# Optimization experiments

Measured on AMD Instinct MI355X. Metric: run time of the kernel, lower is better.

Reference implementation:

```python
import jax, jax.numpy as jnp
import numpy as np

K = 20  # neighbors per point (module default)


def _knn_idx(x, k):
    # x: [N, d] -> indices of k nearest points (self included, as in torch_cluster.knn)
    d2 = jnp.sum(x * x, axis=-1)
    dist = d2[:, None] + d2[None, :] - 2.0 * (x @ x.T)  # [N, N] squared distances
    _, idx = jax.lax.top_k(-dist, k)  # smallest distances
    return idx  # [N, k]


def _mlp(h, layers):
    # layers: list of (W, b, relu_flag); BN is identity (eval mode, fresh running stats)
    for W, b, relu in layers:
        h = h @ W + b
        if relu:
            h = jax.nn.relu(h)
    return h


def _dynamic_edge_conv(x, layers, k=K):
    # x: [B, N, d]; dynamic kNN graph per graph, edge feat [x_i, x_j - x_i], MLP, max-aggr
    idx = jax.vmap(lambda xx: _knn_idx(jax.lax.stop_gradient(xx), k))(x)  # [B, N, k]
    xj = jax.vmap(lambda xx, ii: xx[ii])(x, idx)  # [B, N, k, d] neighbor gather
    xi = x[:, :, None, :]
    feat = jnp.concatenate([jnp.broadcast_to(xi, xj.shape), xj - xi], axis=-1)  # [B,N,k,2d]
    return jnp.max(_mlp(feat, layers), axis=2)  # [B, N, d_out]


def setup_inputs() -> dict:
    key = jax.random.key(0)
    ks = jax.random.split(key, 20)
    s = 0.05
    B, N, PD, OUT = 8, 4096, 2, 10
    f32 = jnp.float32

    def w(k, shape):
        return jax.random.normal(k, shape, dtype=f32) * s

    return {
        "data": jax.random.normal(ks[0], (B, N, PD), dtype=f32),
        # conv1 MLP: [2*PD, 64, 64, 64]
        "c1w1": w(ks[1], (2 * PD, 64)), "c1b1": jnp.zeros((64,), f32),
        "c1w2": w(ks[2], (64, 64)),     "c1b2": jnp.zeros((64,), f32),
        "c1w3": w(ks[3], (64, 64)),     "c1b3": jnp.zeros((64,), f32),
        # conv2 MLP: [2*64, 128]
        "c2w1": w(ks[4], (128, 128)),   "c2b1": jnp.zeros((128,), f32),
        # lin1: 192 -> 1024
        "lin1_w": w(ks[5], (192, 1024)), "lin1_b": jnp.zeros((1024,), f32),
        # head MLP: [1024, 512, 256, OUT]
        "mw1": w(ks[6], (1024, 512)), "mb1": jnp.zeros((512,), f32),
        "mw2": w(ks[7], (512, 256)),  "mb2": jnp.zeros((256,), f32),
        "mw3": w(ks[8], (256, OUT)),  "mb3": jnp.zeros((OUT,), f32),
    }


def reference(data, c1w1, c1b1, c1w2, c1b2, c1w3, c1b3, c2w1, c2b1,
              lin1_w, lin1_b, mw1, mb1, mw2, mb2, mw3, mb3):
    # DynamicEdgeConv 1: MLP([4,64,64,64]) (plain last layer)
    x1 = _dynamic_edge_conv(data, [(c1w1, c1b1, True), (c1w2, c1b2, True), (c1w3, c1b3, False)])
    # DynamicEdgeConv 2: MLP([128,128]) (single plain linear)
    x2 = _dynamic_edge_conv(x1, [(c2w1, c2b1, False)])
    out = jnp.concatenate([x1, x2], axis=-1) @ lin1_w + lin1_b  # [B, N, 1024]
    out = jnp.max(out, axis=1)  # global max pool over points -> [B, 1024]
    out = _mlp(out, [(mw1, mb1, True), (mw2, mb2, True), (mw3, mb3, False)])
    return jax.nn.log_softmax(out, axis=1)
```

## Files before the change

### kernel.cpp

```cpp
#include <hip/hip_runtime.h>
#include <math.h>

#define DEVI static __device__ __forceinline__
#define F_INF __builtin_inff()

typedef short bf16x8 __attribute__((ext_vector_type(8)));
typedef float floatx4 __attribute__((ext_vector_type(4)));
typedef unsigned short ub16x4 __attribute__((ext_vector_type(4)));

DEVI unsigned short bf16rne(float f)
{
    unsigned u = __float_as_uint(f);
    unsigned r = (u + 0x7FFFu + ((u >> 16) & 1u)) >> 16;
    return (unsigned short)r;
}
DEVI float bf16tof(unsigned short h) { return __uint_as_float(((unsigned)h) << 16); }

DEVI bool lexlt(float d, int i, float dr, int ir)
{
    return (d < dr) || (d == dr && i < ir);
}

DEVI void insert20(float* bd, int* bi, float d, int i)
{
#pragma unroll
    for (int j = 19; j >= 1; --j) {
        bool lt  = d < bd[j];
        bool ltp = d < bd[j - 1];
        float nd = ltp ? bd[j - 1] : d;
        int   ni = ltp ? bi[j - 1] : i;
        bd[j] = lt ? nd : bd[j];
        bi[j] = lt ? ni : bi[j];
    }
    bool lt0 = d < bd[0];
    bd[0] = lt0 ? d : bd[0];
    bi[0] = lt0 ? i : bi[0];
}

DEVI void insert_tiered(float* bd, int* bi, float d, int i)
{
    if (__all(!(d < bd[15]))) {
#pragma unroll
        for (int j = 19; j >= 17; --j) {
            bool lt  = d < bd[j];
            bool ltp = d < bd[j - 1];
            float nd = ltp ? bd[j - 1] : d;
            int   ni = ltp ? bi[j - 1] : i;
            bd[j] = lt ? nd : bd[j];
            bi[j] = lt ? ni : bi[j];
        }
        bool lt16 = d < bd[16];
        bd[16] = lt16 ? d : bd[16];
        bi[16] = lt16 ? i : bi[16];
    } else if (__all(!(d < bd[7]))) {
#pragma unroll
        for (int j = 19; j >= 9; --j) {
            bool lt  = d < bd[j];
            bool ltp = d < bd[j - 1];
            float nd = ltp ? bd[j - 1] : d;
            int   ni = ltp ? bi[j - 1] : i;
            bd[j] = lt ? nd : bd[j];
            bi[j] = lt ? ni : bi[j];
        }
        bool lt8 = d < bd[8];
        bd[8] = lt8 ? d : bd[8];
        bi[8] = lt8 ? i : bi[8];
    } else {
        insert20(bd, bi, d, i);
    }
}

DEVI void flushT(float* bd, int* bi, float d, int i, int e, int cnt)
{
    bool want = (e < cnt) && (d < bd[19]);
    if (__any(want))
        insert_tiered(bd, bi, want ? d : F_INF, want ? i : 0x7FFFFFFF);
}

#define FLUSH() do { \
    flushT(bd, bi, a0, j0, 0, cnt); \
    flushT(bd, bi, a1, j1, 1, cnt); \
    flushT(bd, bi, a2, j2, 2, cnt); \
    flushT(bd, bi, a3, j3, 3, cnt); \
    cnt = 0; thr = bd[19]; \
} while (0)

#define APPEND(dv, civ) do { \
    bool pass_ = (dv) < thr; \
    if (pass_) { \
        a0 = (cnt == 0) ? (dv) : a0; j0 = (cnt == 0) ? (civ) : j0; \
        a1 = (cnt == 1) ? (dv) : a1; j1 = (cnt == 1) ? (civ) : j1; \
        a2 = (cnt == 2) ? (dv) : a2; j2 = (cnt == 2) ? (civ) : j2; \
        a3 = (cnt == 3) ? (dv) : a3; j3 = (cnt == 3) ? (civ) : j3; \
        ++cnt; \
    } \
    if (__any(cnt == 4)) { FLUSH(); } \
} while (0)

__global__ __launch_bounds__(64) void k_merge8(const float* __restrict__ partD,
                                               const int* __restrict__ partI,
                                               int* __restrict__ idxo)
{
    const size_t LS = 655360;
    int q = blockIdx.x * 64 + threadIdx.x;
    const float* rd = partD + (size_t)q * 20;
    const int*   ri = partI + (size_t)q * 20;
    int p0 = 0, p1 = 0, p2 = 0, p3 = 0, p4 = 0, p5 = 0, p6 = 0, p7 = 0;
    int* op = idxo + (size_t)q * 20;
    for (int r = 0; r < 20; ++r) {
        float d0 = rd[p0],            d1 = rd[LS + p1];
        float d2v = rd[2 * LS + p2],  d3 = rd[3 * LS + p3];
        float d4 = rd[4 * LS + p4],   d5 = rd[5 * LS + p5];
        float d6 = rd[6 * LS + p6],   d7 = rd[7 * LS + p7];
        int   i0 = ri[p0],            i1 = ri[LS + p1];
        int   i2 = ri[2 * LS + p2],   i3 = ri[3 * LS + p3];
        int   i4v = ri[4 * LS + p4],  i5 = ri[5 * LS + p5];
        int   i6 = ri[6 * LS + p6],   i7 = ri[7 * LS + p7];
        bool wA = lexlt(d1, i1, d0, i0);   float dA = wA ? d1 : d0; int iA = wA ? i1 : i0; int sA = wA ? 1 : 0;
        bool wB = lexlt(d3, i3, d2v, i2);  float dB = wB ? d3 : d2v; int iB = wB ? i3 : i2; int sB = wB ? 3 : 2;
        bool wC = lexlt(d5, i5, d4, i4v);  float dC = wC ? d5 : d4; int iC = wC ? i5 : i4v; int sC = wC ? 5 : 4;
        bool wD = lexlt(d7, i7, d6, i6);   float dD = wD ? d7 : d6; int iD = wD ? i7 : i6; int sD = wD ? 7 : 6;
        bool wE = lexlt(dB, iB, dA, iA);   float dE = wE ? dB : dA; int iE = wE ? iB : iA; int sE = wE ? sB : sA;
        bool wF = lexlt(dD, iD, dC, iC);   float dF = wF ? dD : dC; int iF = wF ? iD : iC; int sF = wF ? sD : sC;
        bool wG = lexlt(dF, iF, dE, iE);   int ig = wG ? iF : iE;   int sg = wG ? sF : sE;
        op[r] = ig;
        p0 += (sg == 0); p1 += (sg == 1); p2 += (sg == 2); p3 += (sg == 3);
        p4 += (sg == 4); p5 += (sg == 5); p6 += (sg == 6); p7 += (sg == 7);
    }
}

__global__ __launch_bounds__(256, 4) void k_knn2d(const float* __restrict__ x,
                                                  float* __restrict__ partD, int* __restrict__ partI)
{
    __shared__ float2 pts[4096];
    int t = threadIdx.x;
    int blk = blockIdx.x;
    int b = blk >> 7;
    int qt = (blk >> 1) & 63;
    int s = blk & 1;
    const float* xb = x + (size_t)b * 4096 * 2;
    for (int f = t; f < 2048; f += 256)
        ((float4*)pts)[f] = ((const float4*)xb)[f];
    __syncthreads();

    int l = t & 63, w = t >> 6;
    int q = qt * 64 + l;
    float2 qp = pts[q];
    float d2i = qp.x * qp.x + qp.y * qp.y;

    float bd[20]; int bi[20];
#pragma unroll
    for (int j = 0; j < 20; ++j) { bd[j] = F_INF; bi[j] = -1; }
    int cnt = 0; float thr = F_INF;
    float a0 = 0, a1 = 0, a2 = 0, a3 = 0;
    int   j0 = 0, j1 = 0, j2 = 0, j3 = 0;

    int m0 = s * 2048 + w * 512;
    for (int m = m0; m < m0 + 512; ++m) {
        float2 p = pts[m];
        float d2j = p.x * p.x + p.y * p.y;
        float dot = qp.x * p.x + qp.y * p.y;
        float dist = (d2i + d2j) - 2.0f * dot;
        APPEND(dist, m);
    }
    FLUSH();

    size_t base = (((size_t)(s * 4 + w)) * 32768 + (b * 4096 + q)) * 20;
#pragma unroll
    for (int k = 0; k < 20; ++k) { partD[base + k] = bd[k]; partI[base + k] = bi[k]; }
}

__global__ void k_prep1(const float* __restrict__ x, const float* __restrict__ w1,
                        const float* __restrict__ b1, float* __restrict__ pm, float* __restrict__ qv)
{
    int tid = blockIdx.x * 256 + threadIdx.x;
    int n = tid >> 6, i = tid & 63;
    float x0 = x[(size_t)n * 2], x1v = x[(size_t)n * 2 + 1];
    float wa = w1[i], wb = w1[64 + i], wc = w1[128 + i], wd = w1[192 + i];
    pm[tid] = fmaf(x0, wa - wc, fmaf(x1v, wb - wd, b1[i]));
    qv[tid] = fmaf(x0, wc, x1v * wd);
}

__global__ __launch_bounds__(256) void k_edge1(const float* __restrict__ pm, const float* __restrict__ q,
                                               const int* __restrict__ idx1,
                                               const float* __restrict__ w2, const float* __restrict__ b2,
                                               const float* __restrict__ w3, const float* __restrict__ b3,
                                               float* __restrict__ x1, float* __restrict__ d2x1)
{
    int t = threadIdx.x;
    int w = t >> 6, l = t & 63;
    int pg = l / 20;
    int k  = l - pg * 20;
    int n0 = blockIdx.x * 12 + w * 3 + pg;
    bool valid = (l < 60) && (n0 < 32768);
    int n = valid ? n0 : 0;
    int b = n >> 12;
    int j = idx1[(size_t)n * 20 + k];
    const float4* pmr = (const float4*)(pm + (size_t)n * 64);
    const float4* qr  = (const float4*)(q + ((size_t)(b * 4096) + j) * 64);

    float h1[64];
#pragma unroll
    for (int i4 = 0; i4 < 16; ++i4) {
        float4 a = pmr[i4], c = qr[i4];
        h1[i4 * 4 + 0] = fmaxf(a.x + c.x, 0.f);
        h1[i4 * 4 + 1] = fmaxf(a.y + c.y, 0.f);
        h1[i4 * 4 + 2] = fmaxf(a.z + c.z, 0.f);
        h1[i4 * 4 + 3] = fmaxf(a.w + c.w, 0.f);
    }
    float h2[64];
#pragma unroll
    for (int o = 0; o < 64; ++o) h2[o] = b2[o];
#pragma unroll
    for (int i = 0; i < 64; ++i) {
        const float* r = w2 + i * 64;
#pragma unroll
        for (int o = 0; o < 64; ++o) h2[o] = fmaf(h1[i], r[o], h2[o]);
    }
#pragma unroll
    for (int o = 0; o < 64; ++o) h2[o] = fmaxf(h2[o], 0.f);

    float h3[64];
#pragma unroll
    for (int o = 0; o < 64; ++o) h3[o] = b3[o];
#pragma unroll
    for (int i = 0; i < 64; ++i) {
        const float* r = w3 + i * 64;
#pragma unroll
        for (int o = 0; o < 64; ++o) h3[o] = fmaf(h2[i], r[o], h3[o]);
    }

    int s16 = (k + 16 < 20) ? (l + 16) : l;
    int s8  = (k + 8  < 20) ? (l + 8)  : l;
    int s4  = (k + 4  < 20) ? (l + 4)  : l;
    int s2  = (k + 2  < 20) ? (l + 2)  : l;
    int s1  = (k + 1  < 20) ? (l + 1)  : l;
#pragma unroll
    for (int o = 0; o < 64; ++o) {
        float v = h3[o];
        v = fmaxf(v, __shfl(v, s16));
        v = fmaxf(v, __shfl(v, s8));
        v = fmaxf(v, __shfl(v, s4));
        v = fmaxf(v, __shfl(v, s2));
        v = fmaxf(v, __shfl(v, s1));
        h3[o] = v;
    }
    if (valid && k == 0) {
        float d2 = 0.f;
#pragma unroll
        for (int o = 0; o < 64; ++o) d2 += h3[o] * h3[o];
        float4* op = (float4*)(x1 + (size_t)n * 64);
#pragma unroll
        for (int i4 = 0; i4 < 16; ++i4)
            op[i4] = make_float4(h3[i4 * 4], h3[i4 * 4 + 1], h3[i4 * 4 + 2], h3[i4 * 4 + 3]);
        d2x1[n] = d2;
    }
}

__global__ __launch_bounds__(256) void k_split(const float* __restrict__ x1,
                                               unsigned short* __restrict__ xi)
{
    int id = blockIdx.x * 256 + threadIdx.x;
    int n = id >> 4, dp = id & 15;
    float4 v = ((const float4*)x1)[id];
    float vv[4] = { v.x, v.y, v.z, v.w };
    ub16x4 h, m, l;
#pragma unroll
    for (int i = 0; i < 4; ++i) {
        float x = vv[i];
        unsigned short hb = bf16rne(x);  float fh = bf16tof(hb);
        float r1 = x - fh;
        unsigned short mb = bf16rne(r1); float fm = bf16tof(mb);
        float r2 = r1 - fm;
        unsigned short lb = bf16rne(r2);
        h[i] = hb; m[i] = mb; l[i] = lb;
    }
    size_t rb = (size_t)n * 192;
    *(ub16x4*)(xi + rb +       dp * 4) = h;
    *(ub16x4*)(xi + rb +  64 + dp * 4) = m;
    *(ub16x4*)(xi + rb + 128 + dp * 4) = l;
}

__global__ __launch_bounds__(256, 4) void k_knn64(const unsigned short* __restrict__ xi,
                                                  const float* __restrict__ d2x1,
                                                  float* __restrict__ partD, int* __restrict__ partI)
{
    __shared__ bf16x8 qlds[1536];
    __shared__ float dlds[4 * 16 * 64];

    int t = threadIdx.x;
    int blk = blockIdx.x;
    int qt = blk >> 4;
    int bb = (blk >> 1) & 7;
    int s  = blk & 1;
    int qbase  = bb * 4096 + qt * 64;
    int cstart = s * 2048;
    int w = t >> 6, l = t & 63;
    int r16 = l & 15, g = l >> 4;

    for (int f = t; f < 1536; f += 256) {
        int lane = f & 63, kc = (f >> 6) & 1, qb = (f >> 7) & 3, pl = f >> 9;
        size_t off = ((size_t)(qbase + qb * 16 + (lane & 15))) * 192 + pl * 64
                   + kc * 32 + 8 * (lane >> 4);
        qlds[f] = *(const bf16x8*)(xi + off);
    }
    float d2ql = d2x1[qbase + l];
    __syncthreads();

    float bd[20]; int bi[20];
#pragma unroll
    for (int j = 0; j < 20; ++j) { bd[j] = F_INF; bi[j] = -1; }
    int cnt = 0; float thr = F_INF;
    float a0 = 0, a1 = 0, a2 = 0, a3 = 0;
    int   j0 = 0, j1 = 0, j2 = 0, j3 = 0;

    const bf16x8* qf = qlds;
    float* myD = dlds + w * 1024;

    for (int T = 0; T < 32; ++T) {
        __syncthreads();
        int csl = cstart + T * 64 + 16 * w;
        int csg = bb * 4096 + csl;

        bf16x8 bh[2], bm[2], blv[2];
#pragma unroll
        for (int kc = 0; kc < 2; ++kc) {
            size_t rb = ((size_t)(csg + r16)) * 192 + kc * 32 + 8 * g;
            bh[kc]  = *(const bf16x8*)(xi + rb);
            bm[kc]  = *(const bf16x8*)(xi + rb + 64);
            blv[kc] = *(const bf16x8*)(xi + rb + 128);
        }
        float d2cv = (l < 16) ? d2x1[csg + l] : 0.f;

        floatx4 acc[4];
#pragma unroll
        for (int qb = 0; qb < 4; ++qb) acc[qb] = (floatx4){0.f, 0.f, 0.f, 0.f};
#pragma unroll
        for (int qb = 0; qb < 4; ++qb)
#pragma unroll
            for (int kc = 0; kc < 2; ++kc) {
                bf16x8 qh_ = qf[((0 * 4 + qb) * 2 + kc) * 64 + l];
                bf16x8 qm_ = qf[((1 * 4 + qb) * 2 + kc) * 64 + l];
                bf16x8 ql_ = qf[((2 * 4 + qb) * 2 + kc) * 64 + l];
                acc[qb] = __builtin_amdgcn_mfma_f32_16x16x32_bf16(qh_, bh[kc],  acc[qb], 0, 0, 0);
                acc[qb] = __builtin_amdgcn_mfma_f32_16x16x32_bf16(qh_, bm[kc],  acc[qb], 0, 0, 0);
                acc[qb] = __builtin_amdgcn_mfma_f32_16x16x32_bf16(qm_, bh[kc],  acc[qb], 0, 0, 0);
                acc[qb] = __builtin_amdgcn_mfma_f32_16x16x32_bf16(qm_, bm[kc],  acc[qb], 0, 0, 0);
                acc[qb] = __builtin_amdgcn_mfma_f32_16x16x32_bf16(qh_, blv[kc], acc[qb], 0, 0, 0);
                acc[qb] = __builtin_amdgcn_mfma_f32_16x16x32_bf16(ql_, bh[kc],  acc[qb], 0, 0, 0);
            }

#pragma unroll
        for (int qb = 0; qb < 4; ++qb) {
            int colp = (qb * 16 + g * 4) ^ ((r16 & 7) << 2);
            *(floatx4*)&myD[r16 * 64 + colp] = acc[qb];
        }

#pragma unroll
        for (int c = 0; c < 16; ++c) {
            float dot = myD[c * 64 + (l ^ ((c & 7) << 2))];
            float d2c = __shfl(d2cv, c);
            float dist = (d2ql + d2c) - 2.0f * dot;
            APPEND(dist, csl + c);
        }
    }
    FLUSH();

    size_t base = (((size_t)(s * 4 + w)) * 32768 + (qbase + l)) * 20;
#pragma unroll
    for (int k = 0; k < 20; ++k) { partD[base + k] = bd[k]; partI[base + k] = bi[k]; }
}

__global__ __launch_bounds__(128) void k_prep2(const float* __restrict__ x1, const float* __restrict__ w,
                                               const float* __restrict__ bias,
                                               float* __restrict__ T, float* __restrict__ V)
{
    __shared__ float xs[8][64];
    int o = threadIdx.x;
    int g = blockIdx.x * 8;
    for (int t = threadIdx.x; t < 512; t += 128) xs[t >> 6][t & 63] = x1[(size_t)g * 64 + t];
    __syncthreads();
    float at[8] = {}, av[8] = {};
    for (int i = 0; i < 64; ++i) {
        float wt = w[i * 128 + o], wv = w[(64 + i) * 128 + o];
#pragma unroll
        for (int p = 0; p < 8; ++p) {
            float xv = xs[p][i];
            at[p] = fmaf(xv, wt, at[p]);
            av[p] = fmaf(xv, wv, av[p]);
        }
    }
    float bo = bias[o];
#pragma unroll
    for (int p = 0; p < 8; ++p) {
        T[(size_t)(g + p) * 128 + o] = at[p] - av[p] + bo;
        V[(size_t)(g + p) * 128 + o] = av[p];
    }
}

__global__ __launch_bounds__(256) void k_edge2(const float* __restrict__ T, const float* __restrict__ V,
                                               const int* __restrict__ idx2, float* __restrict__ x2)
{
    int t = threadIdx.x;
    int p = t >> 5, oc = t & 31;
    int n = blockIdx.x * 8 + p;
    int b = n >> 12;
    const int* ip = idx2 + (size_t)n * 20;
    float4 mx = make_float4(-F_INF, -F_INF, -F_INF, -F_INF);
    for (int k = 0; k < 20; ++k) {
        int j = ip[k];
        float4 v = ((const float4*)(V + ((size_t)(b * 4096) + j) * 128))[oc];
        mx.x = fmaxf(mx.x, v.x); mx.y = fmaxf(mx.y, v.y);
        mx.z = fmaxf(mx.z, v.z); mx.w = fmaxf(mx.w, v.w);
    }
    float4 tv = ((const float4*)(T + (size_t)n * 128))[oc];
    float4 r = make_float4(tv.x + mx.x, tv.y + mx.y, tv.z + mx.z, tv.w + mx.w);
    ((float4*)(x2 + (size_t)n * 128))[oc] = r;
}

__global__ __launch_bounds__(256) void k_lin1max(const float* __restrict__ x1, const float* __restrict__ x2,
                                                 const float* __restrict__ w, const float* __restrict__ bias,
                                                 float* __restrict__ partial)
{
    __shared__ float fs[32][192];
    int blk = blockIdx.x;
    int b = blk >> 7, c = blk & 127;
    int base_n = b * 4096 + c * 32;
    for (int t = threadIdx.x; t < 2048; t += 256) {
        int n = t >> 6, i = t & 63;
        fs[n][i] = x1[(size_t)(base_n + n) * 64 + i];
    }
    for (int t = threadIdx.x; t < 4096; t += 256) {
        int n = t >> 7, i = t & 127;
        fs[n][64 + i] = x2[(size_t)(base_n + n) * 128 + i];
    }
    __syncthreads();

    float acc[32][4];
#pragma unroll
    for (int n = 0; n < 32; ++n)
#pragma unroll
        for (int oo = 0; oo < 4; ++oo) acc[n][oo] = 0.f;

    for (int i4 = 0; i4 < 48; ++i4) {
        float wv[4][4];
#pragma unroll
        for (int r = 0; r < 4; ++r)
#pragma unroll
            for (int oo = 0; oo < 4; ++oo)
                wv[r][oo] = w[(size_t)(i4 * 4 + r) * 1024 + oo * 256 + threadIdx.x];
#pragma unroll
        for (int n = 0; n < 32; ++n) {
            float4 f = *(const float4*)&fs[n][i4 * 4];
#pragma unroll
            for (int oo = 0; oo < 4; ++oo) {
                acc[n][oo] = fmaf(f.x, wv[0][oo], acc[n][oo]);
                acc[n][oo] = fmaf(f.y, wv[1][oo], acc[n][oo]);
                acc[n][oo] = fmaf(f.z, wv[2][oo], acc[n][oo]);
                acc[n][oo] = fmaf(f.w, wv[3][oo], acc[n][oo]);
            }
        }
    }
#pragma unroll
    for (int oo = 0; oo < 4; ++oo) {
        int o = oo * 256 + threadIdx.x;
        float m = -F_INF;
#pragma unroll
        for (int n = 0; n < 32; ++n) m = fmaxf(m, acc[n][oo]);
        partial[((size_t)b * 128 + c) * 1024 + o] = m + bias[o];
    }
}

__global__ void k_red(const float* __restrict__ partial, float* __restrict__ pooled)
{
    int t = blockIdx.x * 256 + threadIdx.x;
    int b = t >> 10, o = t & 1023;
    float m = -F_INF;
    for (int c = 0; c < 128; ++c) m = fmaxf(m, partial[((size_t)b * 128 + c) * 1024 + o]);
    pooled[t] = m;
}

__global__ __launch_bounds__(256) void k_fc1(const float* __restrict__ pooled, const float* __restrict__ w,
                                             const float* __restrict__ bias, float* __restrict__ g1)
{
    __shared__ float ps[8 * 1024];
    for (int t = threadIdx.x; t < 8192; t += 256) ps[t] = pooled[t];
    __syncthreads();
    int o = blockIdx.x * 256 + threadIdx.x;
    float acc[8] = {};
    for (int i4 = 0; i4 < 256; ++i4) {
        float w0 = w[(size_t)(i4 * 4 + 0) * 512 + o];
        float w1v = w[(size_t)(i4 * 4 + 1) * 512 + o];
        float w2v = w[(size_t)(i4 * 4 + 2) * 512 + o];
        float w3v = w[(size_t)(i4 * 4 + 3) * 512 + o];
#pragma unroll
        for (int bb = 0; bb < 8; ++bb) {
            float4 f = *(const float4*)&ps[bb * 1024 + i4 * 4];
            acc[bb] = fmaf(f.x, w0, fmaf(f.y, w1v, fmaf(f.z, w2v, fmaf(f.w, w3v, acc[bb]))));
        }
    }
    float bo = bias[o];
#pragma unroll
    for (int bb = 0; bb < 8; ++bb) g1[bb * 512 + o] = fmaxf(acc[bb] + bo, 0.f);
}

__global__ __launch_bounds__(256) void k_fc2(const float* __restrict__ g1, const float* __restrict__ w,
                                             const float* __restrict__ bias, float* __restrict__ g2)
{
    __shared__ float gs[8 * 512];
    for (int t = threadIdx.x; t < 4096; t += 256) gs[t] = g1[t];
    __syncthreads();
    int o = threadIdx.x;
    float acc[8] = {};
    for (int i4 = 0; i4 < 128; ++i4) {
        float w0 = w[(size_t)(i4 * 4 + 0) * 256 + o];
        float w1v = w[(size_t)(i4 * 4 + 1) * 256 + o];
        float w2v = w[(size_t)(i4 * 4 + 2) * 256 + o];
        float w3v = w[(size_t)(i4 * 4 + 3) * 256 + o];
#pragma unroll
        for (int bb = 0; bb < 8; ++bb) {
            float4 f = *(const float4*)&gs[bb * 512 + i4 * 4];
            acc[bb] = fmaf(f.x, w0, fmaf(f.y, w1v, fmaf(f.z, w2v, fmaf(f.w, w3v, acc[bb]))));
        }
    }
    float bo = bias[o];
#pragma unroll
    for (int bb = 0; bb < 8; ++bb) g2[bb * 256 + o] = fmaxf(acc[bb] + bo, 0.f);
}

__global__ void k_fc3sm(const float* __restrict__ g2, const float* __restrict__ w,
                        const float* __restrict__ bias, float* __restrict__ out)
{
    int t = threadIdx.x;
    int b = t >> 4, l = t & 15;
    float lg = -F_INF;
    if (l < 10) {
        float a = bias[l];
        for (int i = 0; i < 256; ++i) a = fmaf(g2[b * 256 + i], w[i * 10 + l], a);
        lg = a;
    }
    float m = lg;
    m = fmaxf(m, __shfl_xor(m, 1, 16));
    m = fmaxf(m, __shfl_xor(m, 2, 16));
    m = fmaxf(m, __shfl_xor(m, 4, 16));
    m = fmaxf(m, __shfl_xor(m, 8, 16));
    float e = (l < 10) ? expf(lg - m) : 0.f;
    float s = e;
    s += __shfl_xor(s, 1, 16);
    s += __shfl_xor(s, 2, 16);
    s += __shfl_xor(s, 4, 16);
    s += __shfl_xor(s, 8, 16);
    if (l < 10) out[b * 10 + l] = (lg - m) - logf(s);
}

extern "C" void kernel_launch(void* const* d_in, const int* in_sizes, int n_in,
                              void* d_out, int out_size, void* d_ws, size_t ws_size,
                              hipStream_t stream)
{
    (void)in_sizes; (void)n_in; (void)out_size; (void)ws_size;
    const float* data  = (const float*)d_in[0];
    const float* c1w1  = (const float*)d_in[1];
    const float* c1b1  = (const float*)d_in[2];
    const float* c1w2  = (const float*)d_in[3];
    const float* c1b2  = (const float*)d_in[4];
    const float* c1w3  = (const float*)d_in[5];
    const float* c1b3  = (const float*)d_in[6];
    const float* c2w1  = (const float*)d_in[7];
    const float* c2b1  = (const float*)d_in[8];
    const float* lin1w = (const float*)d_in[9];
    const float* lin1b = (const float*)d_in[10];
    const float* mw1   = (const float*)d_in[11];
    const float* mb1   = (const float*)d_in[12];
    const float* mw2   = (const float*)d_in[13];
    const float* mb2   = (const float*)d_in[14];
    const float* mw3   = (const float*)d_in[15];
    const float* mb3   = (const float*)d_in[16];
    float* ws  = (float*)d_ws;
    int*   wsi = (int*)d_ws;
    float* out = (float*)d_out;

    const size_t OFF_IDX1 = 0;
    const size_t OFF_IDX2 = 0;
    const size_t OFF_X1   = 655360;
    const size_t OFF_D2   = 2752512;
    const size_t OFF_PM   = 2785280;
    const size_t OFF_Q    = 4882432;
    const size_t OFF_PD   = 2785280;
    const size_t OFF_PI   = 8028160;
    const size_t OFF_T    = 2785280;
    const size_t OFF_V    = 6979584;
    const size_t OFF_X2   = 11173888;
    const size_t OFF_PART = 15368192;
    const size_t OFF_POOL = 16416768;
    const size_t OFF_G1   = 16424960;
    const size_t OFF_G2   = 16429056;
    const size_t OFF_XI   = 13271040;

    k_knn2d<<<1024, 256, 0, stream>>>(data, ws + OFF_PD, wsi + OFF_PI);
    k_merge8<<<512, 64, 0, stream>>>(ws + OFF_PD, wsi + OFF_PI, wsi + OFF_IDX1);
    k_prep1<<<8192, 256, 0, stream>>>(data, c1w1, c1b1, ws + OFF_PM, ws + OFF_Q);
    k_edge1<<<2731, 256, 0, stream>>>(ws + OFF_PM, ws + OFF_Q, wsi + OFF_IDX1,
                                      c1w2, c1b2, c1w3, c1b3, ws + OFF_X1, ws + OFF_D2);
    k_split<<<2048, 256, 0, stream>>>(ws + OFF_X1, (unsigned short*)(ws + OFF_XI));
    k_knn64<<<1024, 256, 0, stream>>>((const unsigned short*)(ws + OFF_XI),
                                      ws + OFF_D2, ws + OFF_PD, wsi + OFF_PI);
    k_merge8<<<512, 64, 0, stream>>>(ws + OFF_PD, wsi + OFF_PI, wsi + OFF_IDX2);
    k_prep2<<<4096, 128, 0, stream>>>(ws + OFF_X1, c2w1, c2b1, ws + OFF_T, ws + OFF_V);
    k_edge2<<<4096, 256, 0, stream>>>(ws + OFF_T, ws + OFF_V, wsi + OFF_IDX2, ws + OFF_X2);
    k_lin1max<<<1024, 256, 0, stream>>>(ws + OFF_X1, ws + OFF_X2, lin1w, lin1b, ws + OFF_PART);
    k_red<<<32, 256, 0, stream>>>(ws + OFF_PART, ws + OFF_POOL);
    k_fc1<<<2, 256, 0, stream>>>(ws + OFF_POOL, mw1, mb1, ws + OFF_G1);
    k_fc2<<<1, 256, 0, stream>>>(ws + OFF_G1, mw2, mb2, ws + OFF_G2);
    k_fc3sm<<<1, 128, 0, stream>>>(ws + OFF_G2, mw3, mb3, out);
}
```

Before: 1.377 ms.

## Fuse bf16 triple-split into edge1 and prefetch next kNN candidate tile

Removes the separate k_split kernel by having k_edge1 write the hi/mid/lo bf16 split of x1 directly from registers, avoiding a launch and a re-read of x1. In k_knn64 the candidate fragments and norms for the next tile are loaded right after the current MFMA block, so global-load latency overlaps with the distance/top-k append work. The prefetch raises register pressure in a kernel with launch bounds 256,4, and the per-lane split store in edge1 is done serially by one lane per point.

New measurement: 1.488 ms. 1.08x slower.

```diff
diff --git a/kernel.cpp b/kernel.cpp
--- a/kernel.cpp
+++ b/kernel.cpp
@@ -185,7 +185,8 @@
                                                const int* __restrict__ idx1,
                                                const float* __restrict__ w2, const float* __restrict__ b2,
                                                const float* __restrict__ w3, const float* __restrict__ b3,
-                                               float* __restrict__ x1, float* __restrict__ d2x1)
+                                               float* __restrict__ x1, float* __restrict__ d2x1,
+                                               unsigned short* __restrict__ xi)
 {
     int t = threadIdx.x;
     int w = t >> 6, l = t & 63;
@@ -254,31 +255,26 @@
         for (int i4 = 0; i4 < 16; ++i4)
             op[i4] = make_float4(h3[i4 * 4], h3[i4 * 4 + 1], h3[i4 * 4 + 2], h3[i4 * 4 + 3]);
         d2x1[n] = d2;
-    }
-}
-
-__global__ __launch_bounds__(256) void k_split(const float* __restrict__ x1,
-                                               unsigned short* __restrict__ xi)
-{
-    int id = blockIdx.x * 256 + threadIdx.x;
-    int n = id >> 4, dp = id & 15;
-    float4 v = ((const float4*)x1)[id];
-    float vv[4] = { v.x, v.y, v.z, v.w };
-    ub16x4 h, m, l;
-#pragma unroll
-    for (int i = 0; i < 4; ++i) {
-        float x = vv[i];
-        unsigned short hb = bf16rne(x);  float fh = bf16tof(hb);
-        float r1 = x - fh;
-        unsigned short mb = bf16rne(r1); float fm = bf16tof(mb);
-        float r2 = r1 - fm;
-        unsigned short lb = bf16rne(r2);
-        h[i] = hb; m[i] = mb; l[i] = lb;
-    }
-    size_t rb = (size_t)n * 192;
-    *(ub16x4*)(xi + rb +       dp * 4) = h;
-    *(ub16x4*)(xi + rb +  64 + dp * 4) = m;
-    *(ub16x4*)(xi + rb + 128 + dp * 4) = l;
+
+        size_t rb = (size_t)n * 192;
+#pragma unroll
+        for (int i4 = 0; i4 < 16; ++i4) {
+            ub16x4 hh, mm, ll;
+#pragma unroll
+            for (int i = 0; i < 4; ++i) {
+                float x = h3[i4 * 4 + i];
+                unsigned short hb = bf16rne(x);  float fh = bf16tof(hb);
+                float r1 = x - fh;
+                unsigned short mb = bf16rne(r1); float fm = bf16tof(mb);
+                float r2 = r1 - fm;
+                unsigned short lb = bf16rne(r2);
+                hh[i] = hb; mm[i] = mb; ll[i] = lb;
+            }
+            *(ub16x4*)(xi + rb +       i4 * 4) = hh;
+            *(ub16x4*)(xi + rb +  64 + i4 * 4) = mm;
+            *(ub16x4*)(xi + rb + 128 + i4 * 4) = ll;
+        }
+    }
 }
 
 __global__ __launch_bounds__(256, 4) void k_knn64(const unsigned short* __restrict__ xi,
@@ -305,7 +301,6 @@
         qlds[f] = *(const bf16x8*)(xi + off);
     }
     float d2ql = d2x1[qbase + l];
-    __syncthreads();
 
     float bd[20]; int bi[20];
 #pragma unroll
@@ -317,12 +312,10 @@
     const bf16x8* qf = qlds;
     float* myD = dlds + w * 1024;
 
-    for (int T = 0; T < 32; ++T) {
-        __syncthreads();
-        int csl = cstart + T * 64 + 16 * w;
-        int csg = bb * 4096 + csl;
-
-        bf16x8 bh[2], bm[2], blv[2];
+    bf16x8 bh[2], bm[2], blv[2];
+    float d2cv;
+    {
+        int csg = bb * 4096 + cstart + 16 * w;
 #pragma unroll
         for (int kc = 0; kc < 2; ++kc) {
             size_t rb = ((size_t)(csg + r16)) * 192 + kc * 32 + 8 * g;
@@ -330,7 +323,13 @@
             bm[kc]  = *(const bf16x8*)(xi + rb + 64);
             blv[kc] = *(const bf16x8*)(xi + rb + 128);
         }
-        float d2cv = (l < 16) ? d2x1[csg + l] : 0.f;
+        d2cv = (l < 16) ? d2x1[csg + l] : 0.f;
+    }
+    __syncthreads();
+
+    for (int T = 0; T < 32; ++T) {
+        __syncthreads();
+        int csl = cstart + T * 64 + 16 * w;
 
         floatx4 acc[4];
 #pragma unroll
@@ -350,6 +349,19 @@
                 acc[qb] = __builtin_amdgcn_mfma_f32_16x16x32_bf16(ql_, bh[kc],  acc[qb], 0, 0, 0);
             }
 
+        float d2cn = 0.f;
+        if (T + 1 < 32) {
+            int csg2 = bb * 4096 + cstart + (T + 1) * 64 + 16 * w;
+#pragma unroll
+            for (int kc = 0; kc < 2; ++kc) {
+                size_t rb = ((size_t)(csg2 + r16)) * 192 + kc * 32 + 8 * g;
+                bh[kc]  = *(const bf16x8*)(xi + rb);
+                bm[kc]  = *(const bf16x8*)(xi + rb + 64);
+                blv[kc] = *(const bf16x8*)(xi + rb + 128);
+            }
+            d2cn = (l < 16) ? d2x1[csg2 + l] : 0.f;
+        }
+
 #pragma unroll
         for (int qb = 0; qb < 4; ++qb) {
             int colp = (qb * 16 + g * 4) ^ ((r16 & 7) << 2);
@@ -363,6 +375,7 @@
             float dist = (d2ql + d2c) - 2.0f * dot;
             APPEND(dist, csl + c);
         }
+        d2cv = d2cn;
     }
     FLUSH();
 
@@ -600,8 +613,8 @@
     k_merge8<<<512, 64, 0, stream>>>(ws + OFF_PD, wsi + OFF_PI, wsi + OFF_IDX1);
     k_prep1<<<8192, 256, 0, stream>>>(data, c1w1, c1b1, ws + OFF_PM, ws + OFF_Q);
     k_edge1<<<2731, 256, 0, stream>>>(ws + OFF_PM, ws + OFF_Q, wsi + OFF_IDX1,
-                                      c1w2, c1b2, c1w3, c1b3, ws + OFF_X1, ws + OFF_D2);
-    k_split<<<2048, 256, 0, stream>>>(ws + OFF_X1, (unsigned short*)(ws + OFF_XI));
+                                      c1w2, c1b2, c1w3, c1b3, ws + OFF_X1, ws + OFF_D2,
+                                      (unsigned short*)(ws + OFF_XI));
     k_knn64<<<1024, 256, 0, stream>>>((const unsigned short*)(ws + OFF_XI),
                                       ws + OFF_D2, ws + OFF_PD, wsi + OFF_PI);
     k_merge8<<<512, 64, 0, stream>>>(ws + OFF_PD, wsi + OFF_PI, wsi + OFF_IDX2);
```
